# Performance work log

Measured on AMD Instinct MI355X. Metric: run time of the kernel, lower is better.

## Reference

```python
import jax, jax.numpy as jnp
import numpy as np

N_NODES = 50000
N_EDGES = 800000
N_GRAPHS = 1000
D_NODE = 92
D_EDGE = 41
D_HID = 128
D_OUT = 1


def _glorot(key, shape):
    fan_in, fan_out = shape[1], shape[0]
    lim = jnp.sqrt(6.0 / (fan_in + fan_out))
    return jax.random.uniform(key, shape, jnp.float32, -lim, lim)


def setup_inputs() -> dict:
    key = jax.random.key(0)
    ks = jax.random.split(key, 16)
    x = jax.random.normal(ks[0], (N_NODES, D_NODE), jnp.float32)
    edge_index = jax.random.randint(ks[1], (2, N_EDGES), 0, N_NODES, jnp.int64)
    edge_attr = jax.random.uniform(ks[2], (N_EDGES, D_EDGE), jnp.float32)
    batch = jnp.sort(jax.random.randint(ks[3], (N_NODES,), 0, N_GRAPHS, jnp.int64))
    z_in = 2 * D_HID + D_EDGE  # CGConv concat dim
    return {
        "x": x, "edge_index": edge_index, "edge_attr": edge_attr, "batch": batch,
        "W_node": _glorot(ks[4], (D_HID, D_NODE)), "b_node": jnp.zeros((D_HID,), jnp.float32),
        "Wf1": _glorot(ks[5], (D_HID, z_in)), "bf1": jnp.zeros((D_HID,), jnp.float32),
        "Ws1": _glorot(ks[6], (D_HID, z_in)), "bs1": jnp.zeros((D_HID,), jnp.float32),
        "Wf2": _glorot(ks[7], (D_HID, z_in)), "bf2": jnp.zeros((D_HID,), jnp.float32),
        "Ws2": _glorot(ks[8], (D_HID, z_in)), "bs2": jnp.zeros((D_HID,), jnp.float32),
        "W1": _glorot(ks[9], (D_HID, D_HID)), "b1": jnp.zeros((D_HID,), jnp.float32),
        "W2": _glorot(ks[10], (D_OUT, D_HID)), "b2": jnp.zeros((D_OUT,), jnp.float32),
    }


def _cgconv(h, src, dst, edge_attr, Wf, bf, Ws, bs):
    # PyG CGConv: z_ij = [x_i, x_j, e_ij]; msg = sigmoid(lin_f(z)) * softplus(lin_s(z))
    # aggr='add' at target i; residual: out = x + aggr
    z = jnp.concatenate([h[dst], h[src], edge_attr], axis=1)  # [E, 2*D_HID + D_EDGE]
    msg = jax.nn.sigmoid(z @ Wf.T + bf) * jax.nn.softplus(z @ Ws.T + bs)  # [E, D_HID]
    agg = jax.ops.segment_sum(msg, dst, num_segments=N_NODES)
    return h + agg


def reference(x, edge_index, edge_attr, batch,
              W_node, b_node, Wf1, bf1, Ws1, bs1, Wf2, bf2, Ws2, bs2,
              W1, b1, W2, b2):
    src, dst = edge_index[0], edge_index[1]  # message flows j(src) -> i(dst)
    h = jax.nn.leaky_relu(x @ W_node.T + b_node)
    h = jax.nn.leaky_relu(_cgconv(h, src, dst, edge_attr, Wf1, bf1, Ws1, bs1))
    atom_embs = jax.nn.leaky_relu(_cgconv(h, src, dst, edge_attr, Wf2, bf2, Ws2, bs2))
    pooled = jax.ops.segment_sum(atom_embs, batch, num_segments=N_GRAPHS)  # [G, D_HID]
    norm = jnp.maximum(jnp.linalg.norm(pooled, axis=1, keepdims=True), 1e-12)
    g = pooled / norm
    g = jax.nn.leaky_relu(g @ W1.T + b1)
    out = g @ W2.T + b2
    return (out, atom_embs)
```

## Files before the change

### kernel.cpp

```cpp
#include <hip/hip_runtime.h>
#include <math.h>

#define NN 50000
#define NE 800000
#define NG 1000
#define DN 92
#define DE 41
#define DH 128

typedef float f32x4 __attribute__((ext_vector_type(4)));
typedef short s16x8 __attribute__((ext_vector_type(8)));
typedef __fp16 f16x2 __attribute__((ext_vector_type(2)));
typedef __fp16 f16x8 __attribute__((ext_vector_type(8)));
typedef float f32x4u __attribute__((ext_vector_type(4), aligned(4)));

#define OFF_A     ((size_t)0)
#define OFF_ABF   ((size_t)6400000)
#define OFF_PI    ((size_t)9600000)
#define OFF_PJ    ((size_t)16000000)
#define OFF_WCATB ((size_t)22400000)
#define OFF_WTE   ((size_t)22465536)
#define OFF_POOL  ((size_t)22481920)
#define OFF_CNT   ((size_t)22609920)
#define OFF_CUR   ((size_t)22659920)
#define OFF_SE    ((size_t)22709920)
#define OFF_SDST  ((size_t)24309920)

__device__ __forceinline__ float leaky(float x) { return x > 0.f ? x : 0.01f * x; }
__device__ __forceinline__ ushort f2bf(float x) {
    uint u = __float_as_uint(x);
    return (ushort)((u + 0x7fffu + ((u >> 16) & 1u)) >> 16);
}
__device__ __forceinline__ ushort f2h(float x) {
    union { __fp16 h; ushort u; } c;
    c.h = (__fp16)x;
    return c.u;
}
__device__ __forceinline__ f16x2 u2h(uint u) {
    union { uint u; f16x2 h; } c;
    c.u = u;
    return c.h;
}

__device__ __forceinline__ float gate(float f, float s) {
    float sg = 1.f / (1.f + __expf(-f));
    float sp = fmaxf(s, 0.f) + __logf(1.f + __expf(-fabsf(s)));
    return sg * sp;
}

__device__ __forceinline__ int xcd_swz(int bid, int nbid) {
    int cpx = nbid >> 3;
    return (bid & 7) * cpx + (bid >> 3);
}

__device__ __forceinline__ f16x8 pack8h(const float* v) {
    union { f16x2 h[4]; f16x8 s; } r;
#pragma unroll
    for (int p = 0; p < 4; p++)
        r.h[p] = __builtin_amdgcn_cvt_pkrtz(v[2 * p], v[2 * p + 1]);
    return r.s;
}
__device__ __forceinline__ uint pkh1(float a, float b) {
    union { f16x2 h; uint u; } c;
    c.h = __builtin_amdgcn_cvt_pkrtz(a, b);
    return c.u;
}
__device__ __forceinline__ uint cvtpk1(float a, float b) {
    uint r;
    asm("v_cvt_pk_bf16_f32 %0, %1, %2" : "=v"(r) : "v"(a), "v"(b));
    return r;
}

__global__ __launch_bounds__(128) void k_node_embed(const float* __restrict__ x,
        const float* __restrict__ Wn, const float* __restrict__ bn,
        float* __restrict__ A, ushort* __restrict__ Abf) {
    __shared__ __align__(16) float xs[16 * DN];
    const int n0 = blockIdx.x * 16;
    const int t = threadIdx.x;
    const float4* xg = (const float4*)(x + (size_t)n0 * DN);
    float4* xs4 = (float4*)xs;
    for (int i = t; i < 16 * DN / 4; i += 128) xs4[i] = xg[i];
    __syncthreads();
    const int o = t;
    float acc[16];
#pragma unroll
    for (int n = 0; n < 16; n++) acc[n] = 0.f;
    const float4* Wr = (const float4*)(Wn + (size_t)o * DN);
    for (int kk = 0; kk < DN / 4; kk++) {
        float4 w = Wr[kk];
#pragma unroll
        for (int n = 0; n < 16; n++) {
            float4 a = ((const float4*)(xs + n * DN))[kk];
            acc[n] = fmaf(w.x, a.x, acc[n]);
            acc[n] = fmaf(w.y, a.y, acc[n]);
            acc[n] = fmaf(w.z, a.z, acc[n]);
            acc[n] = fmaf(w.w, a.w, acc[n]);
        }
    }
    float b = bn[o];
#pragma unroll
    for (int n = 0; n < 16; n++) {
        float v = leaky(acc[n] + b);
        A[(size_t)(n0 + n) * DH + o] = v;
        Abf[(size_t)(n0 + n) * DH + o] = f2bf(v);
    }
}

__global__ __launch_bounds__(128) void k_pack_wcatb(const float* __restrict__ Wf1,
        const float* __restrict__ Ws1, const float* __restrict__ Wf2,
        const float* __restrict__ Ws2, ushort* __restrict__ Wcatb) {
    int b = blockIdx.x;
    int l = b >> 9, row = b & 511;
    int cb = row >> 7, o = row & 127;
    const float* src;
    if (l == 0) src = (cb < 2) ? Wf1 : Ws1;
    else        src = (cb < 2) ? Wf2 : Ws2;
    int koff = (cb & 1) * 128;
    Wcatb[(size_t)b * 128 + threadIdx.x] = f2bf(src[(size_t)o * 297 + koff + threadIdx.x]);
}

__global__ __launch_bounds__(64) void k_pack_wte(const float* __restrict__ Wf1,
        const float* __restrict__ Ws1, const float* __restrict__ Wf2,
        const float* __restrict__ Ws2, ushort* __restrict__ Wte) {
    int n = blockIdx.x, layer = blockIdx.y, k = threadIdx.x;
    int c = n >> 1, g = n & 1;
    const float* W = layer ? (g ? Ws2 : Wf2) : (g ? Ws1 : Wf1);
    float v = (k < DE) ? W[(size_t)c * 297 + 256 + k] : 0.f;
    Wte[((size_t)(layer * 256 + n)) * 64 + k] = f2h(v);
}

__global__ __launch_bounds__(256) void k_hist(const int* __restrict__ ei,
        int* __restrict__ cnt) {
    int e = blockIdx.x * 256 + threadIdx.x;
    atomicAdd(&cnt[ei[NE + e]], 1);
}

__global__ __launch_bounds__(1024) void k_scan(const int* __restrict__ cnt,
        int* __restrict__ cur) {
    __shared__ int part[1024];
    const int t = threadIdx.x;
    const int lo = t * 49, hi = min(lo + 49, NN);
    int s = 0;
    for (int i = lo; i < hi; i++) s += cnt[i];
    part[t] = s;
    __syncthreads();
    for (int off = 1; off < 1024; off <<= 1) {
        int u = (t >= off) ? part[t - off] : 0;
        __syncthreads();
        part[t] += u;
        __syncthreads();
    }
    int run = part[t] - s;
    for (int i = lo; i < hi; i++) { int c = cnt[i]; cur[i] = run; run += c; }
}

__global__ __launch_bounds__(256) void k_scatter(const int* __restrict__ ei,
        int* __restrict__ cur, uint2* __restrict__ se, int* __restrict__ sdst) {
    int e = blockIdx.x * 256 + threadIdx.x;
    int src = ei[e], dst = ei[NE + e];
    int pos = atomicAdd(&cur[dst], 1);
    se[pos] = make_uint2((uint)src, (uint)e);
    sdst[pos] = dst;
}

__global__ __launch_bounds__(256) void k_gemm_P2(const ushort* __restrict__ Abf,
        const ushort* __restrict__ Wcatb, const float* __restrict__ bf,
        const float* __restrict__ bs, ushort* __restrict__ Pi,
        ushort* __restrict__ Pj) {
    __shared__ ushort Alds[32 * 136];
    __shared__ ushort OTi[32 * 264];
    __shared__ ushort OTj[32 * 264];
    const int n0 = blockIdx.x * 32;
    const int t = threadIdx.x;
    const int cb = t >> 6, l = t & 63, m16 = l & 15, g = l >> 4;

    const uint4* Ag = (const uint4*)Abf;
#pragma unroll
    for (int p = 0; p < 2; p++) {
        int row = (t >> 4) + p * 16;
        int node = n0 + row;
        uint4 v = make_uint4(0u, 0u, 0u, 0u);
        if (node < NN) v = Ag[(size_t)node * 16 + (t & 15)];
        *(uint4*)(Alds + row * 136 + (t & 15) * 8) = v;
    }
    __syncthreads();

    const ushort* Bw = Wcatb + (size_t)cb * 128 * 128;
    f32x4 acc[2][8];
#pragma unroll
    for (int mt = 0; mt < 2; mt++)
#pragma unroll
        for (int nt = 0; nt < 8; nt++) acc[mt][nt] = (f32x4){0.f, 0.f, 0.f, 0.f};

    for (int ks = 0; ks < 4; ks++) {
        s16x8 bfr[8];
#pragma unroll
        for (int nt = 0; nt < 8; nt++)
            bfr[nt] = *(const s16x8*)(Bw + ((size_t)(nt * 16 + m16)) * 128 + ks * 32 + g * 8);
        s16x8 afr[2];
#pragma unroll
        for (int mt = 0; mt < 2; mt++)
            afr[mt] = *(const s16x8*)(Alds + (mt * 16 + m16) * 136 + ks * 32 + g * 8);
#pragma unroll
        for (int mt = 0; mt < 2; mt++)
#pragma unroll
            for (int nt = 0; nt < 8; nt++)
                acc[mt][nt] = __builtin_amdgcn_mfma_f32_16x16x32_bf16(
                    afr[mt], bfr[nt], acc[mt][nt], 0, 0, 0);
    }

    float bias[8];
#pragma unroll
    for (int nt = 0; nt < 8; nt++) bias[nt] = 0.f;
    if (cb == 0) {
#pragma unroll
        for (int nt = 0; nt < 8; nt++) bias[nt] = bf[nt * 16 + m16];
    } else if (cb == 2) {
#pragma unroll
        for (int nt = 0; nt < 8; nt++) bias[nt] = bs[nt * 16 + m16];
    }
    ushort* OT = (cb & 1) ? OTj : OTi;
    const int sel = cb >> 1;
#pragma unroll
    for (int mt = 0; mt < 2; mt++)
#pragma unroll
        for (int nt = 0; nt < 8; nt++)
#pragma unroll
            for (int r = 0; r < 4; r++)
                OT[(mt * 16 + g * 4 + r) * 264 + (nt * 16 + m16) * 2 + sel] =
                    f2h(acc[mt][nt][r] + bias[nt]);
    __syncthreads();
#pragma unroll
    for (int p = 0; p < 4; p++) {
        int idx = t + p * 256;
        int row = idx >> 5, col8 = idx & 31;
        int node = n0 + row;
        if (node < NN) {
            *(uint4*)(Pi + (size_t)node * 256 + col8 * 8) = *(const uint4*)(OTi + row * 264 + col8 * 8);
            *(uint4*)(Pj + (size_t)node * 256 + col8 * 8) = *(const uint4*)(OTj + row * 264 + col8 * 8);
        }
    }
}

__global__ __launch_bounds__(256) void k_edge(const ushort* __restrict__ Pi,
        const ushort* __restrict__ Pj, const uint2* __restrict__ se,
        const int* __restrict__ sdst, const float* __restrict__ ea,
        const ushort* __restrict__ Wte, float* __restrict__ A) {
    __shared__ ushort Elds[32 * 264];
    const int t = threadIdx.x, w = t >> 6, l = t & 63;
    const int bid = xcd_swz(blockIdx.x, gridDim.x);
    const int e0 = bid * 32;
    const int m16 = l & 15, g = l >> 4;

    const uint* PiU = (const uint*)Pi;
    const uint* PjU = (const uint*)Pj;
    const int base = e0 + w * 8;
    uint mysrc = se[base + (l & 7)].x;
    int  mydst = sdst[base + (l & 7)];
    int dsts[8];
    uint pj0a[8], pj1a[8];
#pragma unroll
    for (int i = 0; i < 8; i++) {
        const int src = __builtin_amdgcn_readlane((int)mysrc, i);
        dsts[i] = __builtin_amdgcn_readlane(mydst, i);
        const uint* pjb = PjU + (size_t)src * 128;
        pj0a[i] = pjb[l];
        pj1a[i] = pjb[64 + l];
    }
    int dcur = dsts[0];
    const uint* pib0 = PiU + (size_t)dcur * 128;
    uint pi0 = pib0[l], pi1 = pib0[64 + l];

    f16x8 bt[4][2];
#pragma unroll
    for (int nt = 0; nt < 4; nt++)
#pragma unroll
        for (int ks = 0; ks < 2; ks++)
            bt[nt][ks] = *(const f16x8*)(Wte + ((size_t)(w * 64 + nt * 16 + m16)) * 64 + ks * 32 + g * 8);

    f16x8 at[2][2];
#pragma unroll
    for (int mt = 0; mt < 2; mt++) {
        uint2 s2 = se[e0 + mt * 16 + m16];
        const float* row = ea + (size_t)s2.y * DE;
        f32x4u q0 = *(const f32x4u*)(row + g * 8);
        f32x4u q1 = *(const f32x4u*)(row + g * 8 + 4);
        float v0[8] = {q0.x, q0.y, q0.z, q0.w, q1.x, q1.y, q1.z, q1.w};
        at[mt][0] = pack8h(v0);
        float v1[8] = {0.f, 0.f, 0.f, 0.f, 0.f, 0.f, 0.f, 0.f};
        if (g == 0) {
            f32x4u q2 = *(const f32x4u*)(row + 32);
            f32x4u q3 = *(const f32x4u*)(row + 36);
            v1[0] = q2.x; v1[1] = q2.y; v1[2] = q2.z; v1[3] = q2.w;
            v1[4] = q3.x; v1[5] = q3.y; v1[6] = q3.z; v1[7] = q3.w;
        } else if (g == 1) {
            v1[0] = row[40];
        }
        at[mt][1] = pack8h(v1);
    }

    f32x4 acc[2][4];
#pragma unroll
    for (int mt = 0; mt < 2; mt++)
#pragma unroll
        for (int nt = 0; nt < 4; nt++)
            acc[mt][nt] = (f32x4){0.f, 0.f, 0.f, 0.f};
#pragma unroll
    for (int ks = 0; ks < 2; ks++)
#pragma unroll
        for (int mt = 0; mt < 2; mt++)
#pragma unroll
            for (int nt = 0; nt < 4; nt++)
                acc[mt][nt] = __builtin_amdgcn_mfma_f32_16x16x32_f16(
                    at[mt][ks], bt[nt][ks], acc[mt][nt], 0, 0, 0);

#pragma unroll
    for (int mt = 0; mt < 2; mt++)
#pragma unroll
        for (int nt = 0; nt < 4; nt++) {
            uint u01 = pkh1(acc[mt][nt][0], acc[mt][nt][1]);
            uint u23 = pkh1(acc[mt][nt][2], acc[mt][nt][3]);
            const int col = w * 64 + nt * 16 + m16;
            const int r0 = mt * 16 + g * 4;
            Elds[(r0 + 0) * 264 + col] = (ushort)u01;
            Elds[(r0 + 1) * 264 + col] = (ushort)(u01 >> 16);
            Elds[(r0 + 2) * 264 + col] = (ushort)u23;
            Elds[(r0 + 3) * 264 + col] = (ushort)(u23 >> 16);
        }
    __syncthreads();

    const uint* ElU = (const uint*)Elds;
    float msg0[8], msg1[8];
#pragma unroll
    for (int i = 0; i < 8; i++) {
        if (dsts[i] != dcur) {
            dcur = dsts[i];
            const uint* pb = PiU + (size_t)dcur * 128;
            pi0 = pb[l];
            pi1 = pb[64 + l];
        }
        uint ev0 = ElU[(w * 8 + i) * 132 + l];
        uint ev1 = ElU[(w * 8 + i) * 132 + 64 + l];
        f16x2 t0 = u2h(pi0) + u2h(pj0a[i]) + u2h(ev0);
        f16x2 t1 = u2h(pi1) + u2h(pj1a[i]) + u2h(ev1);
        msg0[i] = gate((float)t0.x, (float)t0.y);
        msg1[i] = gate((float)t1.x, (float)t1.y);
    }
    float c0 = msg0[0], c1 = msg1[0];
    int dprev = dsts[0];
#pragma unroll
    for (int i = 1; i < 8; i++) {
        if (dsts[i] == dprev) { c0 += msg0[i]; c1 += msg1[i]; }
        else {
            atomicAdd(A + (size_t)dprev * DH + l, c0);
            atomicAdd(A + (size_t)dprev * DH + 64 + l, c1);
            c0 = msg0[i]; c1 = msg1[i]; dprev = dsts[i];
        }
    }
    atomicAdd(A + (size_t)dprev * DH + l, c0);
    atomicAdd(A + (size_t)dprev * DH + 64 + l, c1);
}

__global__ __launch_bounds__(256) void k_act(float* __restrict__ A,
        ushort* __restrict__ Abf) {
    int i = blockIdx.x * 256 + threadIdx.x;
    float4* A4 = (float4*)A;
    float4 v = A4[i];
    v.x = leaky(v.x); v.y = leaky(v.y); v.z = leaky(v.z); v.w = leaky(v.w);
    A4[i] = v;
    ((uint2*)Abf)[i] = make_uint2(cvtpk1(v.x, v.y), cvtpk1(v.z, v.w));
}

__global__ __launch_bounds__(256) void k_finalize(const float* __restrict__ A,
        const int* __restrict__ batch, float* __restrict__ embs,
        float* __restrict__ pooled) {
    int idx = blockIdx.x * 256 + threadIdx.x;
    int n = idx >> 7, o = idx & 127;
    float v = leaky(A[idx]);
    embs[idx] = v;
    atomicAdd(pooled + (size_t)batch[n] * DH + o, v);
}

__global__ __launch_bounds__(128) void k_head(const float* __restrict__ pooled,
        const float* __restrict__ W1, const float* __restrict__ b1,
        const float* __restrict__ W2, const float* __restrict__ b2,
        float* __restrict__ out) {
    __shared__ __align__(16) float gl[128];
    __shared__ float red[2];
    const int g = blockIdx.x, o = threadIdx.x;
    const int l = o & 63, wid = o >> 6;
    float p = pooled[(size_t)g * DH + o];
    float v = p * p;
#pragma unroll
    for (int off = 32; off >= 1; off >>= 1) v += __shfl_xor(v, off);
    if (l == 0) red[wid] = v;
    __syncthreads();
    float nrm = fmaxf(sqrtf(red[0] + red[1]), 1e-12f);
    float gv = p / nrm;
    gl[o] = gv;
    __syncthreads();
    float gm = b1[o];
    const float4* Wr = (const float4*)(W1 + (size_t)o * DH);
    const float4* gl4 = (const float4*)gl;
    for (int kk = 0; kk < 32; kk++) {
        float4 w = Wr[kk]; float4 a = gl4[kk];
        gm = fmaf(w.x, a.x, gm); gm = fmaf(w.y, a.y, gm);
        gm = fmaf(w.z, a.z, gm); gm = fmaf(w.w, a.w, gm);
    }
    gm = leaky(gm);
    float c = gm * W2[o];
#pragma unroll
    for (int off = 32; off >= 1; off >>= 1) c += __shfl_xor(c, off);
    __syncthreads();
    if (l == 0) red[wid] = c;
    __syncthreads();
    if (o == 0) out[g] = red[0] + red[1] + b2[0];
}

extern "C" void kernel_launch(void* const* d_in, const int* in_sizes, int n_in,
                              void* d_out, int out_size, void* d_ws, size_t ws_size,
                              hipStream_t stream) {
    const float* x    = (const float*)d_in[0];
    const int*   ei   = (const int*)d_in[1];
    const float* ea   = (const float*)d_in[2];
    const int*   batch= (const int*)d_in[3];
    const float* Wn   = (const float*)d_in[4];
    const float* bn   = (const float*)d_in[5];
    const float* Wf1  = (const float*)d_in[6];
    const float* bf1  = (const float*)d_in[7];
    const float* Ws1  = (const float*)d_in[8];
    const float* bs1  = (const float*)d_in[9];
    const float* Wf2  = (const float*)d_in[10];
    const float* bf2  = (const float*)d_in[11];
    const float* Ws2  = (const float*)d_in[12];
    const float* bs2  = (const float*)d_in[13];
    const float* W1   = (const float*)d_in[14];
    const float* b1   = (const float*)d_in[15];
    const float* W2   = (const float*)d_in[16];
    const float* b2   = (const float*)d_in[17];

    float* ws      = (float*)d_ws;
    float*  A      = ws + OFF_A;
    ushort* Abf    = (ushort*)(ws + OFF_ABF);
    ushort* Pi     = (ushort*)(ws + OFF_PI);
    ushort* Pj     = (ushort*)(ws + OFF_PJ);
    ushort* Wcatb  = (ushort*)(ws + OFF_WCATB);
    ushort* Wte    = (ushort*)(ws + OFF_WTE);
    float*  pooled = ws + OFF_POOL;
    int*    cnt    = (int*)(ws + OFF_CNT);
    int*    cur    = (int*)(ws + OFF_CUR);
    uint2*  se     = (uint2*)(ws + OFF_SE);
    int*    sdst   = (int*)(ws + OFF_SDST);
    float* out     = (float*)d_out;
    float* embs    = out + NG;

    hipMemsetAsync(pooled, 0, (size_t)NG * DH * sizeof(float), stream);
    hipMemsetAsync(cnt, 0, (size_t)NN * sizeof(int), stream);
    k_pack_wcatb<<<1024, 128, 0, stream>>>(Wf1, Ws1, Wf2, Ws2, Wcatb);
    k_pack_wte<<<dim3(256, 2), 64, 0, stream>>>(Wf1, Ws1, Wf2, Ws2, Wte);
    k_node_embed<<<NN / 16, 128, 0, stream>>>(x, Wn, bn, A, Abf);

    k_hist<<<NE / 256, 256, 0, stream>>>(ei, cnt);
    k_scan<<<1, 1024, 0, stream>>>(cnt, cur);
    k_scatter<<<NE / 256, 256, 0, stream>>>(ei, cur, se, sdst);

    k_gemm_P2<<<(NN + 31) / 32, 256, 0, stream>>>(Abf, Wcatb, bf1, bs1, Pi, Pj);
    k_edge<<<NE / 32, 256, 0, stream>>>(Pi, Pj, se, sdst, ea, Wte, A);
    k_act<<<(NN * DH / 4) / 256, 256, 0, stream>>>(A, Abf);

    k_gemm_P2<<<(NN + 31) / 32, 256, 0, stream>>>(Abf, Wcatb + (size_t)512 * 128, bf2, bs2, Pi, Pj);
    k_edge<<<NE / 32, 256, 0, stream>>>(Pi, Pj, se, sdst, ea, Wte + (size_t)256 * 64, A);

    k_finalize<<<NN * DH / 256, 256, 0, stream>>>(A, batch, embs, pooled);
    k_head<<<NG, 128, 0, stream>>>(pooled, W1, b1, W2, b2, out);
}
```

Before: 677.9 us.

## Split edge kernel work across 8 waves, each handling half the columns

The edge kernel goes from 4 to 8 waves per block. Each wave pair shares 8 edges and each wave covers one 64-column half, so the per-wave MFMA tiles, B-fragment registers and gather/atomic work are halved. Pi rows are now loaded per edge rather than reused when consecutive destinations repeat, which adds some redundant gathers. The aim is lower register pressure and more memory-level parallelism for the gather-heavy edge phase.

```diff
diff --git a/kernel.cpp b/kernel.cpp
--- a/kernel.cpp
+++ b/kernel.cpp
@@ -242,7 +242,7 @@
     }
 }
 
-__global__ __launch_bounds__(256) void k_edge(const ushort* __restrict__ Pi,
+__global__ __launch_bounds__(512) void k_edge(const ushort* __restrict__ Pi,
         const ushort* __restrict__ Pj, const uint2* __restrict__ se,
         const int* __restrict__ sdst, const float* __restrict__ ea,
         const ushort* __restrict__ Wte, float* __restrict__ A) {
@@ -254,29 +254,27 @@
 
     const uint* PiU = (const uint*)Pi;
     const uint* PjU = (const uint*)Pj;
-    const int base = e0 + w * 8;
+    const int h = w & 1, g2 = w >> 1;
+    const int base = e0 + g2 * 8;
+    const int co = h * 64 + l;
     uint mysrc = se[base + (l & 7)].x;
     int  mydst = sdst[base + (l & 7)];
     int dsts[8];
-    uint pj0a[8], pj1a[8];
+    uint pja[8], pia[8];
 #pragma unroll
     for (int i = 0; i < 8; i++) {
         const int src = __builtin_amdgcn_readlane((int)mysrc, i);
         dsts[i] = __builtin_amdgcn_readlane(mydst, i);
-        const uint* pjb = PjU + (size_t)src * 128;
-        pj0a[i] = pjb[l];
-        pj1a[i] = pjb[64 + l];
-    }
-    int dcur = dsts[0];
-    const uint* pib0 = PiU + (size_t)dcur * 128;
-    uint pi0 = pib0[l], pi1 = pib0[64 + l];
-
-    f16x8 bt[4][2];
-#pragma unroll
-    for (int nt = 0; nt < 4; nt++)
+        pja[i] = PjU[(size_t)src * 128 + co];
+        pia[i] = PiU[(size_t)dsts[i] * 128 + co];
+    }
+
+    f16x8 bt[2][2];
+#pragma unroll
+    for (int nt = 0; nt < 2; nt++)
 #pragma unroll
         for (int ks = 0; ks < 2; ks++)
-            bt[nt][ks] = *(const f16x8*)(Wte + ((size_t)(w * 64 + nt * 16 + m16)) * 64 + ks * 32 + g * 8);
+            bt[nt][ks] = *(const f16x8*)(Wte + ((size_t)(w * 32 + nt * 16 + m16)) * 64 + ks * 32 + g * 8);
 
     f16x8 at[2][2];
 #pragma unroll
@@ -299,28 +297,28 @@
         at[mt][1] = pack8h(v1);
     }
 
-    f32x4 acc[2][4];
+    f32x4 acc[2][2];
 #pragma unroll
     for (int mt = 0; mt < 2; mt++)
 #pragma unroll
-        for (int nt = 0; nt < 4; nt++)
+        for (int nt = 0; nt < 2; nt++)
             acc[mt][nt] = (f32x4){0.f, 0.f, 0.f, 0.f};
 #pragma unroll
     for (int ks = 0; ks < 2; ks++)
 #pragma unroll
         for (int mt = 0; mt < 2; mt++)
 #pragma unroll
-            for (int nt = 0; nt < 4; nt++)
+            for (int nt = 0; nt < 2; nt++)
                 acc[mt][nt] = __builtin_amdgcn_mfma_f32_16x16x32_f16(
                     at[mt][ks], bt[nt][ks], acc[mt][nt], 0, 0, 0);
 
 #pragma unroll
     for (int mt = 0; mt < 2; mt++)
 #pragma unroll
-        for (int nt = 0; nt < 4; nt++) {
+        for (int nt = 0; nt < 2; nt++) {
             uint u01 = pkh1(acc[mt][nt][0], acc[mt][nt][1]);
             uint u23 = pkh1(acc[mt][nt][2], acc[mt][nt][3]);
-            const int col = w * 64 + nt * 16 + m16;
+            const int col = w * 32 + nt * 16 + m16;
             const int r0 = mt * 16 + g * 4;
             Elds[(r0 + 0) * 264 + col] = (ushort)u01;
             Elds[(r0 + 1) * 264 + col] = (ushort)(u01 >> 16);
@@ -330,35 +328,24 @@
     __syncthreads();
 
     const uint* ElU = (const uint*)Elds;
-    float msg0[8], msg1[8];
+    float msg[8];
 #pragma unroll
     for (int i = 0; i < 8; i++) {
-        if (dsts[i] != dcur) {
-            dcur = dsts[i];
-            const uint* pb = PiU + (size_t)dcur * 128;
-            pi0 = pb[l];
-            pi1 = pb[64 + l];
+        uint ev = ElU[(g2 * 8 + i) * 132 + co];
+        f16x2 t0 = u2h(pia[i]) + u2h(pja[i]) + u2h(ev);
+        msg[i] = gate((float)t0.x, (float)t0.y);
+    }
+    float c0 = msg[0];
+    int dprev = dsts[0];
+#pragma unroll
+    for (int i = 1; i < 8; i++) {
+        if (dsts[i] == dprev) { c0 += msg[i]; }
+        else {
+            atomicAdd(A + (size_t)dprev * DH + co, c0);
+            c0 = msg[i]; dprev = dsts[i];
         }
-        uint ev0 = ElU[(w * 8 + i) * 132 + l];
-        uint ev1 = ElU[(w * 8 + i) * 132 + 64 + l];
-        f16x2 t0 = u2h(pi0) + u2h(pj0a[i]) + u2h(ev0);
-        f16x2 t1 = u2h(pi1) + u2h(pj1a[i]) + u2h(ev1);
-        msg0[i] = gate((float)t0.x, (float)t0.y);
-        msg1[i] = gate((float)t1.x, (float)t1.y);
-    }
-    float c0 = msg0[0], c1 = msg1[0];
-    int dprev = dsts[0];
-#pragma unroll
-    for (int i = 1; i < 8; i++) {
-        if (dsts[i] == dprev) { c0 += msg0[i]; c1 += msg1[i]; }
-        else {
-            atomicAdd(A + (size_t)dprev * DH + l, c0);
-            atomicAdd(A + (size_t)dprev * DH + 64 + l, c1);
-            c0 = msg0[i]; c1 = msg1[i]; dprev = dsts[i];
-        }
-    }
-    atomicAdd(A + (size_t)dprev * DH + l, c0);
-    atomicAdd(A + (size_t)dprev * DH + 64 + l, c1);
+    }
+    atomicAdd(A + (size_t)dprev * DH + co, c0);
 }
 
 __global__ __launch_bounds__(256) void k_act(float* __restrict__ A,
@@ -465,11 +452,11 @@
     k_scatter<<<NE / 256, 256, 0, stream>>>(ei, cur, se, sdst);
 
     k_gemm_P2<<<(NN + 31) / 32, 256, 0, stream>>>(Abf, Wcatb, bf1, bs1, Pi, Pj);
-    k_edge<<<NE / 32, 256, 0, stream>>>(Pi, Pj, se, sdst, ea, Wte, A);
+    k_edge<<<NE / 32, 512, 0, stream>>>(Pi, Pj, se, sdst, ea, Wte, A);
     k_act<<<(NN * DH / 4) / 256, 256, 0, stream>>>(A, Abf);
 
     k_gemm_P2<<<(NN + 31) / 32, 256, 0, stream>>>(Abf, Wcatb + (size_t)512 * 128, bf2, bs2, Pi, Pj);
-    k_edge<<<NE / 32, 256, 0, stream>>>(Pi, Pj, se, sdst, ea, Wte + (size_t)256 * 64, A);
+    k_edge<<<NE / 32, 512, 0, stream>>>(Pi, Pj, se, sdst, ea, Wte + (size_t)256 * 64, A);
 
     k_finalize<<<NN * DH / 256, 256, 0, stream>>>(A, batch, embs, pooled);
     k_head<<<NG, 128, 0, stream>>>(pooled, W1, b1, W2, b2, out);
```

Result: slower. 788.9 us (+16.4%).
